# Kernel optimization log

Measured on AMD Instinct MI355X. Metric: run time of the kernel, lower is better.

The kernel has to match this reference:

```python
import jax, jax.numpy as jnp
import numpy as np

B, T, F = 8, 8192, 1024
H, O = 256, 2


def setup_inputs() -> dict:
    key = jax.random.key(0)
    ks = jax.random.split(key, 12)
    s = 0.02
    return {
        "bags": jax.random.normal(ks[0], (B, T, F), dtype=jnp.float32),
        "mask": jnp.zeros((B, T), dtype=bool),
        "W1": jax.random.normal(ks[1], (F, H), dtype=jnp.float32) * s,
        "b1": jnp.zeros((H,), dtype=jnp.float32),
        "Wv": jax.random.normal(ks[2], (H, H), dtype=jnp.float32) * s,
        "bv": jnp.zeros((H,), dtype=jnp.float32),
        "Wu": jax.random.normal(ks[3], (H, H), dtype=jnp.float32) * s,
        "bu": jnp.zeros((H,), dtype=jnp.float32),
        "ww": jax.random.normal(ks[4], (H, 1), dtype=jnp.float32) * s,
        "bw": jnp.zeros((1,), dtype=jnp.float32),
        "Wc": jax.random.normal(ks[5], (H, O), dtype=jnp.float32) * s,
        "bc": jnp.zeros((O,), dtype=jnp.float32),
    }


def reference(bags, mask, W1, b1, Wv, bv, Wu, bu, ww, bw, Wc, bc):
    # Feature projection + ReLU (dropout is identity in eval mode)
    h = jax.nn.relu(jnp.einsum("btf,fh->bth", bags, W1) + b1)  # (B,T,H)
    # Gated attention
    a_v = jnp.tanh(jnp.einsum("bth,hk->btk", h, Wv) + bv)
    a_u = jax.nn.sigmoid(jnp.einsum("bth,hk->btk", h, Wu) + bu)
    attn_logits = (jnp.einsum("bth,ho->bto", a_v * a_u, ww) + bw)[..., 0]  # (B,T)
    attn_logits = jnp.where(mask, -jnp.inf, attn_logits)
    attn = jax.nn.softmax(attn_logits, axis=1)  # (B,T)
    # Weighted aggregation over tiles
    slide_repr = jnp.einsum("bt,bth->bh", attn, h)  # (B,H)
    logits = slide_repr @ Wc + bc  # (B,O)
    return logits
```

## Files before the change

### kernel.cpp

```cpp
#include <hip/hip_runtime.h>
#include <math.h>

#define BB 8
#define TT 8192
#define FF 1024
#define HH 256
#define MT 64
#define NBLK ((BB*TT)/MT)
#define PBAG (TT/MT)
#define PSTR 260

typedef __attribute__((ext_vector_type(8))) short bf16x8;
typedef __attribute__((ext_vector_type(4))) float f32x4;

__device__ __forceinline__ float b2f(unsigned short s) {
    union { unsigned u; float f; } v; v.u = ((unsigned)s) << 16; return v.f;
}
__device__ __forceinline__ unsigned short f2b(float f) {
    union { float f; unsigned u; } v; v.f = f;
    unsigned u = v.u;
    return (unsigned short)((u + 0x7fffu + ((u >> 16) & 1u)) >> 16);
}
__device__ __forceinline__ unsigned pk2(float a, float b) {
    return (unsigned)f2b(a) | ((unsigned)f2b(b) << 16);
}

__global__ __launch_bounds__(256)
void mil_prep(const float* __restrict__ W1,
              const float* __restrict__ Wv,
              const float* __restrict__ Wu,
              unsigned short* __restrict__ W1f,
              unsigned short* __restrict__ Wvf,
              unsigned short* __restrict__ Wuf) {
    __shared__ unsigned short T[64 * 264];
    const int b = blockIdx.x;
    const int t = threadIdx.x;
    if (b < 64) {
        const int w = b >> 4, kb = b & 15;
#pragma unroll
        for (int i = 0; i < 4; ++i) {
            int f = t + i * 256;
            int r = f >> 4, c4 = (f & 15) * 4;
            float4 v = *(const float4*)(W1 + (size_t)(kb * 64 + r) * 256 + w * 64 + c4);
            T[(c4 + 0) * 72 + r] = f2b(v.x);
            T[(c4 + 1) * 72 + r] = f2b(v.y);
            T[(c4 + 2) * 72 + r] = f2b(v.z);
            T[(c4 + 3) * 72 + r] = f2b(v.w);
        }
        __syncthreads();
#pragma unroll
        for (int i = 0; i < 2; ++i) {
            int c = t + i * 256;
            int fl = c >> 6;
            int k0i = fl >> 2, ni = fl & 3;
            int lane = c & 63, l15 = lane & 15, q = lane >> 4;
            *(uint4*)(W1f + ((size_t)(w * 16 + kb) * 8 + fl) * 512 + lane * 8) =
                *(const uint4*)&T[(ni * 16 + l15) * 72 + k0i * 32 + q * 8];
        }
    } else {
        const int m = (b - 64) >> 2;
        const int w = (b - 64) & 3;
        const float* src = m ? Wu : Wv;
        unsigned short* dst = m ? Wuf : Wvf;
#pragma unroll
        for (int i = 0; i < 16; ++i) {
            int f = t + i * 256;
            int r = f >> 4, c4 = (f & 15) * 4;
            float4 v = *(const float4*)(src + (size_t)r * 256 + w * 64 + c4);
            T[(c4 + 0) * 264 + r] = f2b(v.x);
            T[(c4 + 1) * 264 + r] = f2b(v.y);
            T[(c4 + 2) * 264 + r] = f2b(v.z);
            T[(c4 + 3) * 264 + r] = f2b(v.w);
        }
        __syncthreads();
#pragma unroll
        for (int i = 0; i < 8; ++i) {
            int c = t + i * 256;
            int fl = c >> 6;
            int nc = fl >> 3, ks = fl & 7;
            int lane = c & 63, l15 = lane & 15, q = lane >> 4;
            *(uint4*)(dst + ((size_t)(w * 4 + nc) * 8 + ks) * 512 + lane * 8) =
                *(const uint4*)&T[(nc * 16 + l15) * 264 + ks * 32 + q * 8];
        }
    }
}

__global__ __launch_bounds__(256, 2)
void mil_fused(const float* __restrict__ bags,
               const float* __restrict__ b1,
               const unsigned short* __restrict__ W1f,
               const unsigned char* __restrict__ mask,
               const float* __restrict__ bv,
               const float* __restrict__ bu,
               const float* __restrict__ ww,
               const float* __restrict__ bwp,
               const unsigned short* __restrict__ Wvf,
               const unsigned short* __restrict__ Wuf,
               float* __restrict__ P) {
    const int tid  = threadIdx.x;
    const int wave = tid >> 6;
    const int lane = tid & 63;
    const int l15  = lane & 15;
    const int quad = lane >> 4;
    const int blk  = blockIdx.x;
    const int bag  = blk >> 7;
    const int trow = (blk & 127) * MT;

    __shared__ unsigned short LB[2 * 64 * 136];
    __shared__ float logits[MT];
    __shared__ float wrow[MT];
    __shared__ float sc[2];

    f32x4 acc[4][4];
#pragma unroll
    for (int mi = 0; mi < 4; ++mi)
#pragma unroll
        for (int ni = 0; ni < 4; ++ni)
            acc[mi][ni] = (f32x4){0.f, 0.f, 0.f, 0.f};

    const float* bagrow = bags + (size_t)blk * MT * FF;
    int fr[8], fc[8];
    float4 pf[8];
#pragma unroll
    for (int i = 0; i < 8; ++i) {
        int f = tid + i * 256;
        fr[i] = f >> 5;
        fc[i] = (f & 31) * 4;
        pf[i] = *(const float4*)(bagrow + (size_t)fr[i] * FF + fc[i]);
    }
    const unsigned short* bs = W1f + (size_t)wave * 16 * 4096;

#pragma unroll 2
    for (int kb2 = 0; kb2 < 8; ++kb2) {
        unsigned short* A = LB + (kb2 & 1) * 8704;
#pragma unroll
        for (int i = 0; i < 8; ++i)
            *(uint2*)&A[fr[i] * 136 + fc[i]] =
                make_uint2(pk2(pf[i].x, pf[i].y), pk2(pf[i].z, pf[i].w));
        __syncthreads();
        bf16x8 bb[16];
#pragma unroll
        for (int f16 = 0; f16 < 16; ++f16)
            bb[f16] = *(const bf16x8*)(bs + (size_t)(kb2 * 2 + (f16 >> 3)) * 4096
                                       + (f16 & 7) * 512 + lane * 8);
        if (kb2 < 7) {
#pragma unroll
            for (int i = 0; i < 8; ++i)
                pf[i] = *(const float4*)(bagrow + (size_t)fr[i] * FF + (kb2 + 1) * 128 + fc[i]);
        }
#pragma unroll
        for (int k0i = 0; k0i < 4; ++k0i) {
            bf16x8 afr[4];
#pragma unroll
            for (int mi = 0; mi < 4; ++mi)
                afr[mi] = *(const bf16x8*)&A[(mi * 16 + l15) * 136 + k0i * 32 + quad * 8];
#pragma unroll
            for (int mi = 0; mi < 4; ++mi)
#pragma unroll
                for (int ni = 0; ni < 4; ++ni)
                    acc[mi][ni] = __builtin_amdgcn_mfma_f32_16x16x32_bf16(afr[mi], bb[k0i * 4 + ni], acc[mi][ni], 0, 0, 0);
        }
    }
    __syncthreads();

    {
        float bbv[4];
#pragma unroll
        for (int ni = 0; ni < 4; ++ni) bbv[ni] = b1[wave * 64 + ni * 16 + l15];
#pragma unroll
        for (int mi = 0; mi < 4; ++mi)
#pragma unroll
            for (int ni = 0; ni < 4; ++ni) {
                int n = wave * 64 + ni * 16 + l15;
#pragma unroll
                for (int r = 0; r < 4; ++r) {
                    int m = mi * 16 + quad * 4 + r;
                    float h = fmaxf(acc[mi][ni][r] + bbv[ni], 0.f);
                    LB[m * 264 + n] = f2b(h);
                }
            }
    }
    if (tid < MT) logits[tid] = 0.f;
    __syncthreads();

    float rsum[4][4];
#pragma unroll
    for (int mi = 0; mi < 4; ++mi)
#pragma unroll
        for (int r = 0; r < 4; ++r) rsum[mi][r] = 0.f;

#pragma unroll 1
    for (int nc = 0; nc < 4; ++nc) {
        const int n = wave * 64 + nc * 16 + l15;
        const unsigned short* vs = Wvf + ((size_t)(wave * 4 + nc) * 8) * 512;
        const unsigned short* us = Wuf + ((size_t)(wave * 4 + nc) * 8) * 512;
        f32x4 av[4], au[4];
#pragma unroll
        for (int mi = 0; mi < 4; ++mi) {
            av[mi] = (f32x4){0.f, 0.f, 0.f, 0.f};
            au[mi] = (f32x4){0.f, 0.f, 0.f, 0.f};
        }
#pragma unroll 2
        for (int ks = 0; ks < 8; ++ks) {
            bf16x8 bvf = *(const bf16x8*)(vs + ks * 512 + lane * 8);
            bf16x8 buf_ = *(const bf16x8*)(us + ks * 512 + lane * 8);
            bf16x8 afr[4];
#pragma unroll
            for (int mi = 0; mi < 4; ++mi)
                afr[mi] = *(const bf16x8*)&LB[(mi * 16 + l15) * 264 + ks * 32 + quad * 8];
#pragma unroll
            for (int mi = 0; mi < 4; ++mi) {
                av[mi] = __builtin_amdgcn_mfma_f32_16x16x32_bf16(afr[mi], bvf, av[mi], 0, 0, 0);
                au[mi] = __builtin_amdgcn_mfma_f32_16x16x32_bf16(afr[mi], buf_, au[mi], 0, 0, 0);
            }
        }
        const float bvn = bv[n], bun = bu[n], wn = ww[n];
#pragma unroll
        for (int mi = 0; mi < 4; ++mi)
#pragma unroll
            for (int r = 0; r < 4; ++r) {
                float xv = av[mi][r] + bvn;
                float xu = au[mi][r] + bun;
                float tv = 2.f * __frcp_rn(1.f + __expf(-2.f * xv)) - 1.f;
                float su = __frcp_rn(1.f + __expf(-xu));
                rsum[mi][r] += tv * su * wn;
            }
    }
#pragma unroll
    for (int mi = 0; mi < 4; ++mi)
#pragma unroll
        for (int r = 0; r < 4; ++r) {
            float s = rsum[mi][r];
            s += __shfl_xor(s, 1);
            s += __shfl_xor(s, 2);
            s += __shfl_xor(s, 4);
            s += __shfl_xor(s, 8);
            if (l15 == 0) atomicAdd(&logits[mi * 16 + quad * 4 + r], s);
        }
    __syncthreads();

    if (tid < MT) {
        float lg = logits[tid] + bwp[0];
        if (mask[bag * TT + trow + tid]) lg = -INFINITY;
        logits[tid] = lg;
    }
    __syncthreads();

    if (wave == 0) {
        float v = logits[lane];
        float mx = v;
#pragma unroll
        for (int off = 1; off < 64; off <<= 1) mx = fmaxf(mx, __shfl_xor(mx, off));
        float w = (mx == -INFINITY) ? 0.f : __expf(v - mx);
        wrow[lane] = w;
        float l = w;
#pragma unroll
        for (int off = 1; off < 64; off <<= 1) l += __shfl_xor(l, off);
        if (lane == 0) { sc[0] = mx; sc[1] = l; }
    }
    __syncthreads();

    float a = 0.f;
#pragma unroll 8
    for (int m = 0; m < MT; ++m)
        a += wrow[m] * b2f(LB[m * 264 + tid]);

    float* rec = P + (size_t)blk * PSTR;
    rec[2 + tid] = a;
    if (tid == 0) { rec[0] = sc[0]; rec[1] = sc[1]; }
}

__global__ void mil_final(const float* __restrict__ P,
                          const float* __restrict__ Wc,
                          const float* __restrict__ bc,
                          float* __restrict__ out) {
    const int bag = blockIdx.x;
    const int tid = threadIdx.x;
    __shared__ float marr[PBAG];
    __shared__ float earr[PBAG];
    __shared__ float red[4];
    __shared__ float wred[8];

    if (tid < PBAG) marr[tid] = P[(size_t)(bag * PBAG + tid) * PSTR + 0];
    __syncthreads();
    if (tid < PBAG) {
        float v = marr[tid];
#pragma unroll
        for (int off = 1; off < 64; off <<= 1) v = fmaxf(v, __shfl_xor(v, off));
        if ((tid & 63) == 0) red[tid >> 6] = v;
    }
    __syncthreads();
    const float M = fmaxf(red[0], red[1]);
    if (tid < PBAG) {
        float e = (marr[tid] == -INFINITY) ? 0.f : __expf(marr[tid] - M);
        earr[tid] = e;
        float le = P[(size_t)(bag * PBAG + tid) * PSTR + 1] * e;
#pragma unroll
        for (int off = 1; off < 64; off <<= 1) le += __shfl_xor(le, off);
        if ((tid & 63) == 0) red[2 + (tid >> 6)] = le;
    }
    __syncthreads();
    const float L = red[2] + red[3];

    float accv = 0.f;
#pragma unroll 4
    for (int i = 0; i < PBAG; ++i)
        accv += earr[i] * P[(size_t)(bag * PBAG + i) * PSTR + 2 + tid];
    const float sr = accv / L;

    float p0 = sr * Wc[tid * 2 + 0];
    float p1 = sr * Wc[tid * 2 + 1];
#pragma unroll
    for (int off = 1; off < 64; off <<= 1) {
        p0 += __shfl_xor(p0, off);
        p1 += __shfl_xor(p1, off);
    }
    if ((tid & 63) == 0) {
        wred[(tid >> 6) * 2 + 0] = p0;
        wred[(tid >> 6) * 2 + 1] = p1;
    }
    __syncthreads();
    if (tid == 0) {
        out[bag * 2 + 0] = wred[0] + wred[2] + wred[4] + wred[6] + bc[0];
        out[bag * 2 + 1] = wred[1] + wred[3] + wred[5] + wred[7] + bc[1];
    }
}

extern "C" void kernel_launch(void* const* d_in, const int* in_sizes, int n_in,
                              void* d_out, int out_size, void* d_ws, size_t ws_size,
                              hipStream_t stream) {
    const float*         bags = (const float*)d_in[0];
    const unsigned char* mask = (const unsigned char*)d_in[1];
    const float*         W1   = (const float*)d_in[2];
    const float*         b1   = (const float*)d_in[3];
    const float*         Wv   = (const float*)d_in[4];
    const float*         bv   = (const float*)d_in[5];
    const float*         Wu   = (const float*)d_in[6];
    const float*         bu   = (const float*)d_in[7];
    const float*         ww   = (const float*)d_in[8];
    const float*         bw   = (const float*)d_in[9];
    const float*         Wc   = (const float*)d_in[10];
    const float*         bc   = (const float*)d_in[11];
    float* out = (float*)d_out;

    char* ws = (char*)d_ws;
    unsigned short* W1f = (unsigned short*)(ws);
    unsigned short* Wvf = (unsigned short*)(ws + 524288);
    unsigned short* Wuf = (unsigned short*)(ws + 655360);
    float*          P   = (float*)(ws + 786432);

    mil_prep<<<72, 256, 0, stream>>>(W1, Wv, Wu, W1f, Wvf, Wuf);
    mil_fused<<<NBLK, 256, 0, stream>>>(bags, b1, W1f, mask, bv, bu, ww, bw, Wvf, Wuf, P);
    mil_final<<<BB, 256, 0, stream>>>(P, Wc, bc, out);
}
```

Before: 430.6 us.

## Fuse final bag reduction into main kernel via last-block atomic counter

Removes the separate mil_final launch: each block bumps a per-bag atomic counter after writing its partial record, and the last block for a bag runs the cross-tile softmax merge and the classifier. Block-to-tile mapping is interleaved across bags, so consecutive blocks work on different bags and each bag's reduction finishes near the end of the grid. This saves one kernel launch and its gap, but adds fences and an atomic per block. Counters are reset in the prep kernel.

New measurement: 515.0 us. 1.2x slower.

```diff
diff --git a/kernel.cpp b/kernel.cpp
--- a/kernel.cpp
+++ b/kernel.cpp
@@ -31,10 +31,12 @@
               const float* __restrict__ Wu,
               unsigned short* __restrict__ W1f,
               unsigned short* __restrict__ Wvf,
-              unsigned short* __restrict__ Wuf) {
+              unsigned short* __restrict__ Wuf,
+              unsigned* __restrict__ cnt) {
     __shared__ unsigned short T[64 * 264];
     const int b = blockIdx.x;
     const int t = threadIdx.x;
+    if (b == 0 && t < BB) cnt[t * 32] = 0u;
     if (b < 64) {
         const int w = b >> 4, kb = b & 15;
 #pragma unroll
@@ -96,20 +98,27 @@
                const float* __restrict__ bwp,
                const unsigned short* __restrict__ Wvf,
                const unsigned short* __restrict__ Wuf,
-               float* __restrict__ P) {
+               const float* __restrict__ Wc,
+               const float* __restrict__ bc,
+               float* __restrict__ P,
+               unsigned* __restrict__ cnt,
+               float* __restrict__ out) {
     const int tid  = threadIdx.x;
     const int wave = tid >> 6;
     const int lane = tid & 63;
     const int l15  = lane & 15;
     const int quad = lane >> 4;
     const int blk  = blockIdx.x;
-    const int bag  = blk >> 7;
-    const int trow = (blk & 127) * MT;
+    const int bag  = blk & 7;
+    const int tile = blk >> 3;
+    const int trow = tile * MT;
+    const int rid  = bag * PBAG + tile;
 
     __shared__ unsigned short LB[2 * 64 * 136];
     __shared__ float logits[MT];
     __shared__ float wrow[MT];
     __shared__ float sc[2];
+    __shared__ unsigned lastFlag;
 
     f32x4 acc[4][4];
 #pragma unroll
@@ -118,7 +127,7 @@
         for (int ni = 0; ni < 4; ++ni)
             acc[mi][ni] = (f32x4){0.f, 0.f, 0.f, 0.f};
 
-    const float* bagrow = bags + (size_t)blk * MT * FF;
+    const float* bagrow = bags + ((size_t)bag * TT + trow) * FF;
     int fr[8], fc[8];
     float4 pf[8];
 #pragma unroll
@@ -265,64 +274,67 @@
     for (int m = 0; m < MT; ++m)
         a += wrow[m] * b2f(LB[m * 264 + tid]);
 
-    float* rec = P + (size_t)blk * PSTR;
+    float* rec = P + (size_t)rid * PSTR;
     rec[2 + tid] = a;
     if (tid == 0) { rec[0] = sc[0]; rec[1] = sc[1]; }
-}
-
-__global__ void mil_final(const float* __restrict__ P,
-                          const float* __restrict__ Wc,
-                          const float* __restrict__ bc,
-                          float* __restrict__ out) {
-    const int bag = blockIdx.x;
-    const int tid = threadIdx.x;
-    __shared__ float marr[PBAG];
-    __shared__ float earr[PBAG];
-    __shared__ float red[4];
-    __shared__ float wred[8];
-
-    if (tid < PBAG) marr[tid] = P[(size_t)(bag * PBAG + tid) * PSTR + 0];
-    __syncthreads();
-    if (tid < PBAG) {
-        float v = marr[tid];
-#pragma unroll
-        for (int off = 1; off < 64; off <<= 1) v = fmaxf(v, __shfl_xor(v, off));
-        if ((tid & 63) == 0) red[tid >> 6] = v;
-    }
-    __syncthreads();
-    const float M = fmaxf(red[0], red[1]);
-    if (tid < PBAG) {
-        float e = (marr[tid] == -INFINITY) ? 0.f : __expf(marr[tid] - M);
-        earr[tid] = e;
-        float le = P[(size_t)(bag * PBAG + tid) * PSTR + 1] * e;
-#pragma unroll
-        for (int off = 1; off < 64; off <<= 1) le += __shfl_xor(le, off);
-        if ((tid & 63) == 0) red[2 + (tid >> 6)] = le;
-    }
-    __syncthreads();
-    const float L = red[2] + red[3];
-
-    float accv = 0.f;
+
+    __threadfence();
+    __syncthreads();
+    if (tid == 0)
+        lastFlag = (atomicAdd(&cnt[bag * 32], 1u) == PBAG - 1) ? 1u : 0u;
+    __syncthreads();
+    if (!lastFlag) return;
+    __threadfence();
+
+    {
+        __shared__ float marr[PBAG];
+        __shared__ float earr[PBAG];
+        __shared__ float red[4];
+        __shared__ float wred[8];
+
+        if (tid < PBAG) marr[tid] = P[(size_t)(bag * PBAG + tid) * PSTR + 0];
+        __syncthreads();
+        if (tid < PBAG) {
+            float v = marr[tid];
+#pragma unroll
+            for (int off = 1; off < 64; off <<= 1) v = fmaxf(v, __shfl_xor(v, off));
+            if ((tid & 63) == 0) red[tid >> 6] = v;
+        }
+        __syncthreads();
+        const float M = fmaxf(red[0], red[1]);
+        if (tid < PBAG) {
+            float e = (marr[tid] == -INFINITY) ? 0.f : __expf(marr[tid] - M);
+            earr[tid] = e;
+            float le = P[(size_t)(bag * PBAG + tid) * PSTR + 1] * e;
+#pragma unroll
+            for (int off = 1; off < 64; off <<= 1) le += __shfl_xor(le, off);
+            if ((tid & 63) == 0) red[2 + (tid >> 6)] = le;
+        }
+        __syncthreads();
+        const float L = red[2] + red[3];
+
+        float accv = 0.f;
 #pragma unroll 4
-    for (int i = 0; i < PBAG; ++i)
-        accv += earr[i] * P[(size_t)(bag * PBAG + i) * PSTR + 2 + tid];
-    const float sr = accv / L;
-
-    float p0 = sr * Wc[tid * 2 + 0];
-    float p1 = sr * Wc[tid * 2 + 1];
-#pragma unroll
-    for (int off = 1; off < 64; off <<= 1) {
-        p0 += __shfl_xor(p0, off);
-        p1 += __shfl_xor(p1, off);
-    }
-    if ((tid & 63) == 0) {
-        wred[(tid >> 6) * 2 + 0] = p0;
-        wred[(tid >> 6) * 2 + 1] = p1;
-    }
-    __syncthreads();
-    if (tid == 0) {
-        out[bag * 2 + 0] = wred[0] + wred[2] + wred[4] + wred[6] + bc[0];
-        out[bag * 2 + 1] = wred[1] + wred[3] + wred[5] + wred[7] + bc[1];
+        for (int i = 0; i < PBAG; ++i)
+            accv += earr[i] * P[(size_t)(bag * PBAG + i) * PSTR + 2 + tid];
+        const float sr = accv / L;
+
+        float p0 = sr * Wc[tid * 2 + 0];
+        float p1 = sr * Wc[tid * 2 + 1];
+#pragma unroll
+        for (int off = 1; off < 64; off <<= 1) {
+            p0 += __shfl_xor(p0, off);
+            p1 += __shfl_xor(p1, off);
+        }
+        if ((tid & 63) == 0) {
+            wred[(tid >> 6) * 2 + 0] = p0;
+            wred[(tid >> 6) * 2 + 1] = p1;
+        }
+        __syncthreads();
+        if (tid == 0) {
+            out[bag * 2 + 0] = wred[0] + wred[2] + wred[4] + wred[6] + bc[0];
+            out[bag * 2 + 1] = wred[1] + wred[3] + wred[5] + wred[7] + bc[1];
+        }
     }
 }
 
@@ -348,8 +360,9 @@
     unsigned short* Wvf = (unsigned short*)(ws + 524288);
     unsigned short* Wuf = (unsigned short*)(ws + 655360);
     float*          P   = (float*)(ws + 786432);
-
-    mil_prep<<<72, 256, 0, stream>>>(W1, Wv, Wu, W1f, Wvf, Wuf);
-    mil_fused<<<NBLK, 256, 0, stream>>>(bags, b1, W1f, mask, bv, bu, ww, bw, Wvf, Wuf, P);
-    mil_final<<<BB, 256, 0, stream>>>(P, Wc, bc, out);
-}
+    unsigned*       cnt = (unsigned*)(ws + 1851392);
+
+    mil_prep<<<72, 256, 0, stream>>>(W1, Wv, Wu, W1f, Wvf, Wuf, cnt);
+    mil_fused<<<NBLK, 256, 0, stream>>>(bags, b1, W1f, mask, bv, bu, ww, bw,
+                                        Wvf, Wuf, Wc, bc, P, cnt, out);
+}
```
